# Kernel optimization log

Measured on AMD Instinct MI355X. Metric: run time of the kernel, lower is better.

## Reference

```python
import jax, jax.numpy as jnp
import numpy as np

B, T, K, H, HID, OUT = 128, 128, 8, 3, 256, 2
LOG_STD_MIN, LOG_STD_MAX = -20.0, 2.0


def setup_inputs() -> dict:
    key = jax.random.key(0)
    ks = jax.random.split(key, 12)
    def lin(k, fan_in, fan_out, scale=0.05):
        return jax.random.normal(k, (fan_in, fan_out), dtype=jnp.float32) * scale
    return {
        "state": jax.random.normal(ks[0], (B, T, K), dtype=jnp.float32),
        "noise": jax.random.normal(ks[1], (B, T, OUT), dtype=jnp.float32),
        "Wq": lin(ks[2], K, H * K),
        "Wk": lin(ks[3], K, H * K),
        "Wv": lin(ks[4], K, H * K),
        "W1": lin(ks[5], H * K + K, HID),
        "b1": jnp.zeros((HID,), jnp.float32),
        "W2": lin(ks[6], HID, HID),
        "b2": jnp.zeros((HID,), jnp.float32),
        "Wmu": jax.random.uniform(ks[7], (HID, OUT), jnp.float32, -0.003, 0.003),
        "bmu": jax.random.uniform(ks[8], (OUT,), jnp.float32, -0.003, 0.003),
        "Wls": jax.random.uniform(ks[9], (HID, OUT), jnp.float32, -0.003, 0.003),
        "bls": jax.random.uniform(ks[10], (OUT,), jnp.float32, -0.003, 0.003),
    }


def reference(state, noise, Wq, Wk, Wv, W1, b1, W2, b2, Wmu, bmu, Wls, bls):
    b, t, k = state.shape
    h = H
    # off-diagonal gather indices: idx[i, m] = m if m < i else m + 1  (j != i, ascending)
    cols = jnp.arange(t - 1)
    idx = cols[None, :] + (cols[None, :] >= jnp.arange(t)[:, None]).astype(jnp.int32)  # [t, t-1]
    # rel_state[b, i, m] = state[b, idx[i, m]] - state[b, i]   -> [b, t, t-1, k]
    rel = state[:, idx, :] - state[:, :, None, :]
    # per-head projections (no bias)
    q = (state @ Wq).reshape(b, t, h, k)                      # [b, t, h, k]
    keys = (rel @ Wk).reshape(b, t, t - 1, h, k)              # [b, t, t-1, h, k]
    vals = (rel @ Wv).reshape(b, t, t - 1, h, k)
    # each query attends over its own t-1 relative keys
    scores = jnp.einsum("bthk,btmhk->bhtm", q, keys) / jnp.sqrt(jnp.float32(k))
    w = jax.nn.softmax(scores, axis=-1)                       # [b, h, t, t-1]
    x = jnp.einsum("bhtm,btmhk->bthk", w, vals).reshape(b, t, h * k)
    x = jnp.concatenate([x, state], axis=-1)                  # [b, t, h*k + k]
    x = jax.nn.relu(x @ W1 + b1)
    x = jax.nn.relu(x @ W2 + b2)
    mu = jnp.tanh(x @ Wmu + bmu)
    log_std = jnp.tanh(x @ Wls + bls)
    log_std = LOG_STD_MIN + 0.5 * (LOG_STD_MAX - LOG_STD_MIN) * (log_std + 1.0)
    std = jnp.exp(log_std)
    z = mu + std * noise                                      # rsample
    action = jnp.tanh(z)
    half_log_2pi = jnp.float32(0.5 * np.log(2.0 * np.pi))
    normal_lp = -0.5 * noise * noise - log_std - half_log_2pi
    log_prob = normal_lp - jnp.log(1.0 - action * action + 1e-7)
    log_prob = jnp.sum(log_prob, axis=-1, keepdims=True)
    return action, log_prob
```

## Files before the change

### kernel.cpp

```cpp
#include <hip/hip_runtime.h>
#include <math.h>

namespace {
constexpr int B_  = 128;
constexpr int T_  = 128;
constexpr int K_  = 8;
constexpr int H_  = 3;
constexpr int HK_ = 24;
constexpr int HID_ = 256;
constexpr int OUT_ = 2;
}

typedef __attribute__((ext_vector_type(8))) short bf16x8;
typedef __attribute__((ext_vector_type(4))) float f32x4;

__device__ inline unsigned short f2bf(float x) {
    unsigned int u = __float_as_uint(x);
    u += 0x7FFFu + ((u >> 16) & 1u);
    return (unsigned short)(u >> 16);
}
__device__ inline float bflo(unsigned int u) { return __uint_as_float(u << 16); }
__device__ inline float bfhi(unsigned int u) { return __uint_as_float(u & 0xFFFF0000u); }

template <int CTRL>
__device__ inline float dpp_add(float v) {
    int t = __builtin_amdgcn_update_dpp(0, __float_as_int(v), CTRL, 0xF, 0xF, true);
    return v + __int_as_float(t);
}
__device__ inline float red8(float v) {
    v = dpp_add<0xB1>(v); v = dpp_add<0x4E>(v); return dpp_add<0x141>(v);
}
__device__ inline float red16(float v) {
    return dpp_add<0x140>(red8(v));
}

__global__ __launch_bounds__(256) void prep_kernel(
    const float* __restrict__ state,
    const float* __restrict__ Wq, const float* __restrict__ Wk,
    const float* __restrict__ Wv,
    const float* __restrict__ W1, const float* __restrict__ W2,
    unsigned short* __restrict__ w1t, unsigned short* __restrict__ w2t,
    unsigned short* __restrict__ kb, unsigned short* __restrict__ vb,
    float* __restrict__ qsc)
{
    __shared__ float wq_s[K_*HK_], wk_s[K_*HK_], wv_s[K_*HK_];
    const int tid = threadIdx.x;
    const int blk = blockIdx.x;

    if (blk < 32) {
        const int k0 = blk * 8;
        unsigned short tmp[8];
        #pragma unroll
        for (int i = 0; i < 8; ++i) tmp[i] = f2bf(W2[(size_t)(k0+i)*HID_ + tid]);
        *(bf16x8*)(w2t + (size_t)tid*256 + k0) = *(const bf16x8*)tmp;
        return;
    }
    if (blk < 36) {
        const int k0 = (blk - 32) * 8;
        unsigned short tmp[8];
        #pragma unroll
        for (int i = 0; i < 8; ++i) tmp[i] = f2bf(W1[(size_t)(k0+i)*HID_ + tid]);
        *(bf16x8*)(w1t + (size_t)tid*32 + k0) = *(const bf16x8*)tmp;
        return;
    }

    const int b = blk - 36;
    if (tid < K_*HK_) { wq_s[tid]=Wq[tid]; wk_s[tid]=Wk[tid]; wv_s[tid]=Wv[tid]; }
    __syncthreads();

    const float* sb = state + (size_t)b*T_*K_;
    if (tid < 128) {
        const int j = tid;
        const float4 s0 = *(const float4*)(sb + j*8);
        const float4 s1 = *(const float4*)(sb + j*8 + 4);
        const float sv[8] = {s0.x,s0.y,s0.z,s0.w,s1.x,s1.y,s1.z,s1.w};
        #pragma unroll
        for (int h = 0; h < H_; ++h) {
            unsigned short kp[8], vp[8];
            #pragma unroll
            for (int k = 0; k < 8; ++k) {
                const int col = h*8 + k;
                float ak = 0.f, av = 0.f;
                #pragma unroll
                for (int m = 0; m < K_; ++m) {
                    ak = fmaf(sv[m], wk_s[m*HK_+col], ak);
                    av = fmaf(sv[m], wv_s[m*HK_+col], av);
                }
                kp[k] = f2bf(ak); vp[k] = f2bf(av);
            }
            const size_t off = ((size_t)(b*H_ + h)*T_ + j) * 8;
            *(bf16x8*)(kb + off) = *(const bf16x8*)kp;
            *(bf16x8*)(vb + off) = *(const bf16x8*)vp;
        }
    } else {
        const int i = tid - 128;
        const float4 s0 = *(const float4*)(sb + i*8);
        const float4 s1 = *(const float4*)(sb + i*8 + 4);
        const float sv[8] = {s0.x,s0.y,s0.z,s0.w,s1.x,s1.y,s1.z,s1.w};
        float q[HK_];
        #pragma unroll
        for (int col = 0; col < HK_; ++col) {
            float aq = 0.f;
            #pragma unroll
            for (int m = 0; m < K_; ++m) aq = fmaf(sv[m], wq_s[m*HK_+col], aq);
            q[col] = aq * 0.35355339059327373f;
        }
        float* qo = qsc + (size_t)(b*T_ + i)*HK_;
        #pragma unroll
        for (int c = 0; c < 6; ++c)
            *(float4*)(qo + c*4) = *(const float4*)&q[c*4];
    }
}

__global__ __launch_bounds__(256) void fused_actor_kernel(
    const float* __restrict__ state,
    const float* __restrict__ noise,
    const unsigned short* __restrict__ kb, const unsigned short* __restrict__ vb,
    const float* __restrict__ qsc,
    const unsigned short* __restrict__ w1t, const float* __restrict__ b1,
    const unsigned short* __restrict__ w2t, const float* __restrict__ b2,
    const float* __restrict__ Wmu, const float* __restrict__ bmu,
    const float* __restrict__ Wls, const float* __restrict__ bls,
    float* __restrict__ out)
{
    __shared__ alignas(16) unsigned short a0b[32][40];
    __shared__ alignas(16) unsigned short x1s[32][264];
    __shared__ alignas(16) float hp[4][32][4];

    const int tid  = threadIdx.x;
    const int b    = blockIdx.x >> 2;
    const int iq   = blockIdx.x & 3;
    const int i0   = iq * 32;
    const int w    = tid >> 6;
    const int lane = tid & 63;

    {
        const int i_sub = lane >> 3, jg = lane & 7;
        #pragma unroll
        for (int p = 0; p < 3; ++p) {
            const int pair = w*3 + p;
            const int h  = pair >> 2;
            const int ig = pair & 3;
            const int il = ig*8 + i_sub;
            const int iglob = i0 + il;
            const float* qp = qsc + (size_t)(b*T_ + iglob)*HK_ + h*8;
            const float4 q0 = *(const float4*)qp;
            const float4 q1 = *(const float4*)(qp + 4);
            const unsigned short* kbase = kb + (size_t)(b*H_ + h)*T_*8;
            const unsigned short* vbase = vb + (size_t)(b*H_ + h)*T_*8;
            float l = 0.f;
            float acc[8] = {0.f,0.f,0.f,0.f,0.f,0.f,0.f,0.f};
            #pragma unroll 4
            for (int t = 0; t < 16; ++t) {
                const int j = t*8 + jg;
                const int4 kk = *(const int4*)(kbase + j*8);
                float s;
                s = q0.x * bflo(kk.x) + q0.y * bfhi(kk.x)
                  + q0.z * bflo(kk.y) + q0.w * bfhi(kk.y)
                  + q1.x * bflo(kk.z) + q1.y * bfhi(kk.z)
                  + q1.z * bflo(kk.w) + q1.w * bfhi(kk.w);
                const float e = (j == iglob) ? 0.f : __expf(s);
                l += e;
                const int4 vv = *(const int4*)(vbase + j*8);
                acc[0] = fmaf(e, bflo(vv.x), acc[0]);
                acc[1] = fmaf(e, bfhi(vv.x), acc[1]);
                acc[2] = fmaf(e, bflo(vv.y), acc[2]);
                acc[3] = fmaf(e, bfhi(vv.y), acc[3]);
                acc[4] = fmaf(e, bflo(vv.z), acc[4]);
                acc[5] = fmaf(e, bfhi(vv.z), acc[5]);
                acc[6] = fmaf(e, bflo(vv.w), acc[6]);
                acc[7] = fmaf(e, bfhi(vv.w), acc[7]);
            }
            l = red8(l);
            #pragma unroll
            for (int k = 0; k < 8; ++k) acc[k] = red8(acc[k]);
            if (jg == 0) {
                const float rl = 1.f / l;
                const int4 vi = *(const int4*)(vbase + iglob*8);
                const float vs[8] = { bflo(vi.x), bfhi(vi.x), bflo(vi.y), bfhi(vi.y),
                                      bflo(vi.z), bfhi(vi.z), bflo(vi.w), bfhi(vi.w) };
                unsigned int r01 = (unsigned int)f2bf(acc[0]*rl - vs[0])
                                 | ((unsigned int)f2bf(acc[1]*rl - vs[1]) << 16);
                unsigned int r23 = (unsigned int)f2bf(acc[2]*rl - vs[2])
                                 | ((unsigned int)f2bf(acc[3]*rl - vs[3]) << 16);
                unsigned int r45 = (unsigned int)f2bf(acc[4]*rl - vs[4])
                                 | ((unsigned int)f2bf(acc[5]*rl - vs[5]) << 16);
                unsigned int r67 = (unsigned int)f2bf(acc[6]*rl - vs[6])
                                 | ((unsigned int)f2bf(acc[7]*rl - vs[7]) << 16);
                int4 rr; rr.x = r01; rr.y = r23; rr.z = r45; rr.w = r67;
                *(int4*)&a0b[il][h*8] = rr;
            }
        }
    }
    {
        const int il = tid >> 3, k = tid & 7;
        a0b[il][HK_ + k] = f2bf(state[(size_t)b*T_*K_ + (i0 + il)*K_ + k]);
    }
    __syncthreads();

    const int lq = (tid >> 4) & 3;
    const int ln = tid & 15;

    {
        const bf16x8 a0 = *(const bf16x8*)&a0b[ln][lq*8];
        const bf16x8 a1 = *(const bf16x8*)&a0b[16+ln][lq*8];
        #pragma unroll
        for (int nt = 0; nt < 4; ++nt) {
            const int n0 = (w*4 + nt)*16;
            const bf16x8 bf = *(const bf16x8*)(w1t + (size_t)(n0+ln)*32 + lq*8);
            const float bias = b1[n0+ln];
            f32x4 c = {bias, bias, bias, bias};
            f32x4 d0 = __builtin_amdgcn_mfma_f32_16x16x32_bf16(a0, bf, c, 0, 0, 0);
            f32x4 d1 = __builtin_amdgcn_mfma_f32_16x16x32_bf16(a1, bf, c, 0, 0, 0);
            #pragma unroll
            for (int r = 0; r < 4; ++r) {
                x1s[lq*4 + r][n0+ln]      = f2bf(fmaxf(d0[r], 0.f));
                x1s[16 + lq*4 + r][n0+ln] = f2bf(fmaxf(d1[r], 0.f));
            }
        }
    }
    __syncthreads();

    f32x4 acc2[2][4];
    #pragma unroll
    for (int nt = 0; nt < 4; ++nt) {
        const float bias = b2[(w*4+nt)*16 + ln];
        f32x4 c = {bias, bias, bias, bias};
        acc2[0][nt] = c; acc2[1][nt] = c;
    }
    #pragma unroll 2
    for (int ks = 0; ks < 8; ++ks) {
        const int k0 = ks*32;
        const bf16x8 a0 = *(const bf16x8*)&x1s[ln][k0 + lq*8];
        const bf16x8 a1 = *(const bf16x8*)&x1s[16+ln][k0 + lq*8];
        #pragma unroll
        for (int nt = 0; nt < 4; ++nt) {
            const bf16x8 bf = *(const bf16x8*)(w2t + (size_t)((w*4+nt)*16+ln)*256 + k0 + lq*8);
            acc2[0][nt] = __builtin_amdgcn_mfma_f32_16x16x32_bf16(a0, bf, acc2[0][nt], 0,0,0);
            acc2[1][nt] = __builtin_amdgcn_mfma_f32_16x16x32_bf16(a1, bf, acc2[1][nt], 0,0,0);
        }
    }

    {
        float p[2][4][4];
        #pragma unroll
        for (int mt = 0; mt < 2; ++mt)
            #pragma unroll
            for (int r = 0; r < 4; ++r)
                #pragma unroll
                for (int o = 0; o < 4; ++o) p[mt][r][o] = 0.f;
        #pragma unroll
        for (int nt = 0; nt < 4; ++nt) {
            const int n = (w*4+nt)*16 + ln;
            const float2 wm = *(const float2*)(Wmu + n*OUT_);
            const float2 wl = *(const float2*)(Wls + n*OUT_);
            #pragma unroll
            for (int mt = 0; mt < 2; ++mt) {
                #pragma unroll
                for (int r = 0; r < 4; ++r) {
                    const float x2 = fmaxf(acc2[mt][nt][r], 0.f);
                    p[mt][r][0] = fmaf(x2, wm.x, p[mt][r][0]);
                    p[mt][r][1] = fmaf(x2, wm.y, p[mt][r][1]);
                    p[mt][r][2] = fmaf(x2, wl.x, p[mt][r][2]);
                    p[mt][r][3] = fmaf(x2, wl.y, p[mt][r][3]);
                }
            }
        }
        #pragma unroll
        for (int mt = 0; mt < 2; ++mt)
            #pragma unroll
            for (int r = 0; r < 4; ++r)
                #pragma unroll
                for (int o = 0; o < 4; ++o)
                    p[mt][r][o] = red16(p[mt][r][o]);
        if (ln == 0) {
            #pragma unroll
            for (int mt = 0; mt < 2; ++mt)
                #pragma unroll
                for (int r = 0; r < 4; ++r) {
                    f32x4 pv = {p[mt][r][0], p[mt][r][1], p[mt][r][2], p[mt][r][3]};
                    *(f32x4*)&hp[w][mt*16 + lq*4 + r][0] = pv;
                }
        }
    }
    __syncthreads();

    if (tid < 32) {
        const int r = tid;
        const int grow = b*T_ + i0 + r;
        float pre[4];
        #pragma unroll
        for (int o = 0; o < 4; ++o)
            pre[o] = hp[0][r][o] + hp[1][r][o] + hp[2][r][o] + hp[3][r][o];
        float lp = 0.f;
        #pragma unroll
        for (int o = 0; o < OUT_; ++o) {
            float mu  = tanhf(pre[o]   + bmu[o]);
            float lsp = tanhf(pre[2+o] + bls[o]);
            float log_std = -20.f + 11.f * (lsp + 1.f);
            float sd = __expf(log_std);
            float n  = noise[(size_t)grow*OUT_ + o];
            float z  = fmaf(sd, n, mu);
            float a  = tanhf(z);
            out[(size_t)grow*OUT_ + o] = a;
            lp += -0.5f*n*n - log_std - 0.91893853320467274f
                  - logf(1.f - a*a + 1e-7f);
        }
        out[(size_t)B_*T_*OUT_ + grow] = lp;
    }
}

extern "C" void kernel_launch(void* const* d_in, const int* in_sizes, int n_in,
                              void* d_out, int out_size, void* d_ws, size_t ws_size,
                              hipStream_t stream)
{
    const float* state = (const float*)d_in[0];
    const float* noise = (const float*)d_in[1];
    const float* Wq  = (const float*)d_in[2];
    const float* Wk  = (const float*)d_in[3];
    const float* Wv  = (const float*)d_in[4];
    const float* W1  = (const float*)d_in[5];
    const float* b1  = (const float*)d_in[6];
    const float* W2  = (const float*)d_in[7];
    const float* b2  = (const float*)d_in[8];
    const float* Wmu = (const float*)d_in[9];
    const float* bmu = (const float*)d_in[10];
    const float* Wls = (const float*)d_in[11];
    const float* bls = (const float*)d_in[12];
    float* out = (float*)d_out;

    unsigned short* w1t = (unsigned short*)d_ws;
    unsigned short* w2t = w1t + 8192;
    unsigned short* kbp = w2t + 65536;
    unsigned short* vbp = kbp + 393216;
    float*          qsp = (float*)(vbp + 393216);

    prep_kernel<<<dim3(164), dim3(256), 0, stream>>>(
        state, Wq, Wk, Wv, W1, W2, w1t, w2t, kbp, vbp, qsp);
    fused_actor_kernel<<<dim3(B_*4), dim3(256), 0, stream>>>(
        state, noise, kbp, vbp, qsp, w1t, b1, w2t, b2, Wmu, bmu, Wls, bls, out);
}
```

Before: 106.9 us.

## Compute K/V/Q projections inside fused kernel in shared memory instead of prep kernel

Moves the per-batch K, V and Q projections out of the prep kernel and into the fused actor kernel, which now builds them in LDS for each block. This removes the global round trip for the bf16 K/V and float Q buffers and shrinks the prep launch to just the weight transposes. In exchange, each of the four blocks per batch recomputes the full K/V projection for all 128 tokens, and the kernel gains an extra sync and more LDS use, which may lower occupancy.

```diff
diff --git a/kernel.cpp b/kernel.cpp
--- a/kernel.cpp
+++ b/kernel.cpp
@@ -28,101 +28,48 @@
     return v + __int_as_float(t);
 }
 __device__ inline float red8(float v) {
-    v = dpp_add<0xB1>(v); v = dpp_add<0x4E>(v); return dpp_add<0x141>(v);
+    v = dpp_add<0xB1>(v);
+    v = dpp_add<0x4E>(v);
+    return dpp_add<0x141>(v);
 }
 __device__ inline float red16(float v) {
     return dpp_add<0x140>(red8(v));
 }
 
 __global__ __launch_bounds__(256) void prep_kernel(
-    const float* __restrict__ state,
-    const float* __restrict__ Wq, const float* __restrict__ Wk,
-    const float* __restrict__ Wv,
     const float* __restrict__ W1, const float* __restrict__ W2,
-    unsigned short* __restrict__ w1t, unsigned short* __restrict__ w2t,
-    unsigned short* __restrict__ kb, unsigned short* __restrict__ vb,
-    float* __restrict__ qsc)
+    unsigned short* __restrict__ w1t, unsigned short* __restrict__ w2t)
 {
-    __shared__ float wq_s[K_*HK_], wk_s[K_*HK_], wv_s[K_*HK_];
-    const int tid = threadIdx.x;
-    const int blk = blockIdx.x;
-
-    if (blk < 32) {
-        const int k0 = blk * 8;
-        unsigned short tmp[8];
-        #pragma unroll
-        for (int i = 0; i < 8; ++i) tmp[i] = f2bf(W2[(size_t)(k0+i)*HID_ + tid]);
-        *(bf16x8*)(w2t + (size_t)tid*256 + k0) = *(const bf16x8*)tmp;
-        return;
-    }
-    if (blk < 36) {
-        const int k0 = (blk - 32) * 8;
-        unsigned short tmp[8];
-        #pragma unroll
-        for (int i = 0; i < 8; ++i) tmp[i] = f2bf(W1[(size_t)(k0+i)*HID_ + tid]);
-        *(bf16x8*)(w1t + (size_t)tid*32 + k0) = *(const bf16x8*)tmp;
-        return;
-    }
-
-    const int b = blk - 36;
-    if (tid < K_*HK_) { wq_s[tid]=Wq[tid]; wk_s[tid]=Wk[tid]; wv_s[tid]=Wv[tid]; }
-    __syncthreads();
-
-    const float* sb = state + (size_t)b*T_*K_;
-    if (tid < 128) {
-        const int j = tid;
-        const float4 s0 = *(const float4*)(sb + j*8);
-        const float4 s1 = *(const float4*)(sb + j*8 + 4);
-        const float sv[8] = {s0.x,s0.y,s0.z,s0.w,s1.x,s1.y,s1.z,s1.w};
-        #pragma unroll
-        for (int h = 0; h < H_; ++h) {
-            unsigned short kp[8], vp[8];
-            #pragma unroll
-            for (int k = 0; k < 8; ++k) {
-                const int col = h*8 + k;
-                float ak = 0.f, av = 0.f;
-                #pragma unroll
-                for (int m = 0; m < K_; ++m) {
-                    ak = fmaf(sv[m], wk_s[m*HK_+col], ak);
-                    av = fmaf(sv[m], wv_s[m*HK_+col], av);
-                }
-                kp[k] = f2bf(ak); vp[k] = f2bf(av);
-            }
-            const size_t off = ((size_t)(b*H_ + h)*T_ + j) * 8;
-            *(bf16x8*)(kb + off) = *(const bf16x8*)kp;
-            *(bf16x8*)(vb + off) = *(const bf16x8*)vp;
-        }
+    const int n = threadIdx.x;
+    unsigned short tmp[8];
+    if (blockIdx.x < 32) {
+        const int k0 = blockIdx.x * 8;
+        #pragma unroll
+        for (int i = 0; i < 8; ++i) tmp[i] = f2bf(W2[(size_t)(k0+i)*HID_ + n]);
+        *(bf16x8*)(w2t + (size_t)n*256 + k0) = *(const bf16x8*)tmp;
     } else {
-        const int i = tid - 128;
-        const float4 s0 = *(const float4*)(sb + i*8);
-        const float4 s1 = *(const float4*)(sb + i*8 + 4);
-        const float sv[8] = {s0.x,s0.y,s0.z,s0.w,s1.x,s1.y,s1.z,s1.w};
-        float q[HK_];
-        #pragma unroll
-        for (int col = 0; col < HK_; ++col) {
-            float aq = 0.f;
-            #pragma unroll
-            for (int m = 0; m < K_; ++m) aq = fmaf(sv[m], wq_s[m*HK_+col], aq);
-            q[col] = aq * 0.35355339059327373f;
-        }
-        float* qo = qsc + (size_t)(b*T_ + i)*HK_;
-        #pragma unroll
-        for (int c = 0; c < 6; ++c)
-            *(float4*)(qo + c*4) = *(const float4*)&q[c*4];
+        const int k0 = (blockIdx.x - 32) * 8;
+        #pragma unroll
+        for (int i = 0; i < 8; ++i) tmp[i] = f2bf(W1[(size_t)(k0+i)*HID_ + n]);
+        *(bf16x8*)(w1t + (size_t)n*32 + k0) = *(const bf16x8*)tmp;
     }
 }
 
 __global__ __launch_bounds__(256) void fused_actor_kernel(
     const float* __restrict__ state,
     const float* __restrict__ noise,
-    const unsigned short* __restrict__ kb, const unsigned short* __restrict__ vb,
-    const float* __restrict__ qsc,
+    const float* __restrict__ Wq, const float* __restrict__ Wk,
+    const float* __restrict__ Wv,
     const unsigned short* __restrict__ w1t, const float* __restrict__ b1,
     const unsigned short* __restrict__ w2t, const float* __restrict__ b2,
     const float* __restrict__ Wmu, const float* __restrict__ bmu,
     const float* __restrict__ Wls, const float* __restrict__ bls,
     float* __restrict__ out)
 {
+    __shared__ float wq_s[K_*HK_], wk_s[K_*HK_], wv_s[K_*HK_];
+    __shared__ alignas(16) unsigned short Kb[H_][T_][8];
+    __shared__ alignas(16) unsigned short Vb[H_][T_][8];
+    __shared__ alignas(16) float Qs[32][HK_];
     __shared__ alignas(16) unsigned short a0b[32][40];
     __shared__ alignas(16) unsigned short x1s[32][264];
     __shared__ alignas(16) float hp[4][32][4];
@@ -133,6 +80,54 @@
     const int i0   = iq * 32;
     const int w    = tid >> 6;
     const int lane = tid & 63;
+    const float* sb = state + (size_t)b*T_*K_;
+
+    if (tid < K_*HK_) { wq_s[tid]=Wq[tid]; wk_s[tid]=Wk[tid]; wv_s[tid]=Wv[tid]; }
+    __syncthreads();
+
+    {
+        const int j = tid >> 1, p = tid & 1;
+        const float4 s0 = *(const float4*)(sb + j*8);
+        const float4 s1 = *(const float4*)(sb + j*8 + 4);
+        const float sv[8] = {s0.x,s0.y,s0.z,s0.w,s1.x,s1.y,s1.z,s1.w};
+        const float* ws = p ? wv_s : wk_s;
+        #pragma unroll
+        for (int h = 0; h < H_; ++h) {
+            unsigned short pk[8];
+            #pragma unroll
+            for (int k = 0; k < 8; ++k) {
+                const int col = h*8 + k;
+                float a = 0.f;
+                #pragma unroll
+                for (int m = 0; m < K_; ++m) a = fmaf(sv[m], ws[m*HK_+col], a);
+                pk[k] = f2bf(a);
+            }
+            unsigned short* dst = p ? &Vb[h][j][0] : &Kb[h][j][0];
+            *(bf16x8*)dst = *(const bf16x8*)pk;
+        }
+        if (p == 0 && j >= i0 && j < i0 + 32) {
+            unsigned short sb16[8];
+            #pragma unroll
+            for (int k = 0; k < 8; ++k) sb16[k] = f2bf(sv[k]);
+            *(bf16x8*)&a0b[j - i0][HK_] = *(const bf16x8*)sb16;
+        }
+    }
+    {
+        const int il = tid >> 3;
+        const int c0 = (tid & 7) * 3;
+        const float4 s0 = *(const float4*)(sb + (i0+il)*8);
+        const float4 s1 = *(const float4*)(sb + (i0+il)*8 + 4);
+        const float sv[8] = {s0.x,s0.y,s0.z,s0.w,s1.x,s1.y,s1.z,s1.w};
+        #pragma unroll
+        for (int cc = 0; cc < 3; ++cc) {
+            const int col = c0 + cc;
+            float aq = 0.f;
+            #pragma unroll
+            for (int m = 0; m < K_; ++m) aq = fmaf(sv[m], wq_s[m*HK_+col], aq);
+            Qs[il][col] = aq * 0.35355339059327373f;
+        }
+    }
+    __syncthreads();
 
     {
         const int i_sub = lane >> 3, jg = lane & 7;
@@ -143,17 +138,14 @@
             const int ig = pair & 3;
             const int il = ig*8 + i_sub;
             const int iglob = i0 + il;
-            const float* qp = qsc + (size_t)(b*T_ + iglob)*HK_ + h*8;
-            const float4 q0 = *(const float4*)qp;
-            const float4 q1 = *(const float4*)(qp + 4);
-            const unsigned short* kbase = kb + (size_t)(b*H_ + h)*T_*8;
-            const unsigned short* vbase = vb + (size_t)(b*H_ + h)*T_*8;
+            const float4 q0 = *(const float4*)&Qs[il][h*8];
+            const float4 q1 = *(const float4*)&Qs[il][h*8+4];
             float l = 0.f;
             float acc[8] = {0.f,0.f,0.f,0.f,0.f,0.f,0.f,0.f};
             #pragma unroll 4
             for (int t = 0; t < 16; ++t) {
                 const int j = t*8 + jg;
-                const int4 kk = *(const int4*)(kbase + j*8);
+                const int4 kk = *(const int4*)&Kb[h][j][0];
                 float s;
                 s = q0.x * bflo(kk.x) + q0.y * bfhi(kk.x)
                   + q0.z * bflo(kk.y) + q0.w * bfhi(kk.y)
@@ -161,7 +153,7 @@
                   + q1.z * bflo(kk.w) + q1.w * bfhi(kk.w);
                 const float e = (j == iglob) ? 0.f : __expf(s);
                 l += e;
-                const int4 vv = *(const int4*)(vbase + j*8);
+                const int4 vv = *(const int4*)&Vb[h][j][0];
                 acc[0] = fmaf(e, bflo(vv.x), acc[0]);
                 acc[1] = fmaf(e, bfhi(vv.x), acc[1]);
                 acc[2] = fmaf(e, bflo(vv.y), acc[2]);
@@ -176,7 +168,7 @@
             for (int k = 0; k < 8; ++k) acc[k] = red8(acc[k]);
             if (jg == 0) {
                 const float rl = 1.f / l;
-                const int4 vi = *(const int4*)(vbase + iglob*8);
+                const int4 vi = *(const int4*)&Vb[h][iglob][0];
                 const float vs[8] = { bflo(vi.x), bfhi(vi.x), bflo(vi.y), bfhi(vi.y),
                                       bflo(vi.z), bfhi(vi.z), bflo(vi.w), bfhi(vi.w) };
                 unsigned int r01 = (unsigned int)f2bf(acc[0]*rl - vs[0])
@@ -191,10 +183,6 @@
                 *(int4*)&a0b[il][h*8] = rr;
             }
         }
-    }
-    {
-        const int il = tid >> 3, k = tid & 7;
-        a0b[il][HK_ + k] = f2bf(state[(size_t)b*T_*K_ + (i0 + il)*K_ + k]);
     }
     __syncthreads();
 
@@ -331,12 +319,8 @@
 
     unsigned short* w1t = (unsigned short*)d_ws;
     unsigned short* w2t = w1t + 8192;
-    unsigned short* kbp = w2t + 65536;
-    unsigned short* vbp = kbp + 393216;
-    float*          qsp = (float*)(vbp + 393216);
-
-    prep_kernel<<<dim3(164), dim3(256), 0, stream>>>(
-        state, Wq, Wk, Wv, W1, W2, w1t, w2t, kbp, vbp, qsp);
+
+    prep_kernel<<<dim3(36), dim3(256), 0, stream>>>(W1, W2, w1t, w2t);
     fused_actor_kernel<<<dim3(B_*4), dim3(256), 0, stream>>>(
-        state, noise, kbp, vbp, qsp, w1t, b1, w2t, b2, Wmu, bmu, Wls, bls, out);
-}
+        state, noise, Wq, Wk, Wv, w1t, b1, w2t, b2, Wmu, bmu, Wls, bls, out);
+}
```

Result: faster. 101.9 us (-4.7%).
